# Kernel optimization log

Measured on AMD Instinct MI355X. Metric: run time of the kernel, lower is better.

Reference implementation:

```python
import jax, jax.numpy as jnp
import numpy as np

S, E, CAP = 4096, 64, 128


def setup_inputs() -> dict:
    key = jax.random.key(0)
    k1, k2 = jax.random.split(key)
    logits = jax.random.normal(k1, (S, E), dtype=jnp.float32)
    noise = jax.random.normal(k2, (S, E), dtype=jnp.float32)
    return {"logits": logits, "noise": noise, "capacity": CAP}


def reference(logits, noise, capacity):
    # logits, noise: [S, E]; capacity: python int
    gates = jax.nn.softmax(logits, axis=1)                      # [S, E]
    num_experts = gates.shape[1]

    # top-1 expert
    indices1_s = jnp.argmax(gates, axis=1)                      # [S]
    mask1 = jax.nn.one_hot(indices1_s, num_experts, dtype=jnp.int32)

    # top-2 expert from noised logits with top-1 masked out
    logits_w_noise = logits + noise
    neg_min = jnp.finfo(logits.dtype).min
    logits_except1 = jnp.where(mask1 > 0, neg_min, logits_w_noise)
    indices2_s = jnp.argmax(logits_except1, axis=1)
    mask2 = jax.nn.one_hot(indices2_s, num_experts, dtype=jnp.int32)

    # capacity locations (running count per expert over tokens)
    locations1 = jnp.cumsum(mask1, axis=0) - 1                  # [S, E]
    locations2 = jnp.cumsum(mask2, axis=0) - 1
    locations2 = locations2 + jnp.sum(mask1, axis=0, keepdims=True)

    # load-balancing aux loss
    me = jnp.mean(gates, axis=0)
    ce = jnp.mean(mask1.astype(logits.dtype), axis=0)
    l_aux = jnp.mean(me * ce) * num_experts * num_experts

    # drop tokens over capacity
    mask1 = mask1 * (locations1 < capacity).astype(mask1.dtype)
    mask2 = mask2 * (locations2 < capacity).astype(mask2.dtype)

    locations1_s = jnp.sum(locations1 * mask1, axis=1)          # [S]
    locations2_s = jnp.sum(locations2 * mask2, axis=1)

    mask1_f = mask1.astype(logits.dtype)
    mask2_f = mask2.astype(logits.dtype)
    gates1_s = jnp.einsum('se,se->s', gates, mask1_f)
    gates2_s = jnp.einsum('se,se->s', gates, mask2_f)
    denom_s = jnp.maximum(gates1_s + gates2_s, jnp.finfo(logits.dtype).eps)
    gates1_s = gates1_s / denom_s
    gates2_s = gates2_s / denom_s

    gates1 = gates1_s[:, None] * mask1_f                        # [S, E]
    gates2 = gates2_s[:, None] * mask2_f

    locations1_sc = jax.nn.one_hot(locations1_s, capacity, dtype=logits.dtype)
    locations2_sc = jax.nn.one_hot(locations2_s, capacity, dtype=logits.dtype)

    combine_weights = (gates1[:, :, None] * locations1_sc[:, None, :]
                       + gates2[:, :, None] * locations2_sc[:, None, :])  # [S, E, C]
    dispatch_mask = combine_weights.astype(bool)
    return l_aux, combine_weights, dispatch_mask
```

## Files before the change

### kernel.cpp

```cpp
#include <hip/hip_runtime.h>
#include <float.h>
#include <math.h>

#define SS 4096
#define EE 64
#define CAPC 128
#define ROW 8192
#define SEC (4096LL * 64 * 128)
#define NGATE 256
#define NFILL 4096
#define TPB_TOK 16

__global__ __launch_bounds__(256) void k1_gate_fill(
    const float* __restrict__ logits,
    const float* __restrict__ noise,
    int*   __restrict__ bc1,
    int*   __restrict__ bc2,
    float* __restrict__ pg,
    int*   __restrict__ tokmeta,
    float2* __restrict__ tokg,
    float* __restrict__ out)
{
    const int tid = threadIdx.x;

    if (blockIdx.x >= NGATE) {
        const int fb = blockIdx.x - NGATE;
        float4* p = (float4*)out + (long)fb * 4096;
        const float4 z = make_float4(0.f, 0.f, 0.f, 0.f);
        #pragma unroll
        for (int i = 0; i < 16; ++i) p[i * 256 + tid] = z;
        if (fb == NFILL - 1 && tid == 0) out[2 * SEC] = 0.f;
        return;
    }

    const int b    = blockIdx.x;
    const int wave = tid >> 6;
    const int lane = tid & 63;

    __shared__ int   s_idx1[TPB_TOK], s_idx2[TPB_TOK];
    __shared__ float s_gate[TPB_TOK][64];

    #pragma unroll
    for (int t4 = 0; t4 < 4; ++t4) {
        const int t = wave * 4 + t4;
        const int s = b * TPB_TOK + t;
        const float l = logits[s * EE + lane];
        const float n = noise [s * EE + lane];

        float v = l; int bi = lane;
        #pragma unroll
        for (int off = 32; off; off >>= 1) {
            float v2 = __shfl_xor(v, off, 64);
            int   i2 = __shfl_xor(bi, off, 64);
            if (v2 > v || (v2 == v && i2 < bi)) { v = v2; bi = i2; }
        }
        const int idx1 = bi;

        float e = expf(l - v);
        float sum = e;
        #pragma unroll
        for (int off = 32; off; off >>= 1) sum += __shfl_xor(sum, off, 64);
        const float gate = e / sum;

        float lw = (lane == idx1) ? -FLT_MAX : (l + n);
        float v2v = lw; int bi2 = lane;
        #pragma unroll
        for (int off = 32; off; off >>= 1) {
            float q  = __shfl_xor(v2v, off, 64);
            int   i2 = __shfl_xor(bi2, off, 64);
            if (q > v2v || (q == v2v && i2 < bi2)) { v2v = q; bi2 = i2; }
        }
        const int idx2 = bi2;

        s_gate[t][lane] = gate;
        const float g1v = __shfl(gate, idx1, 64);
        const float g2v = __shfl(gate, idx2, 64);
        if (lane == 0) {
            s_idx1[t] = idx1;
            s_idx2[t] = idx2;
            tokg[s] = make_float2(g1v, g2v);
        }
    }
    __syncthreads();

    if (tid < 64) {
        int c1 = 0, c2 = 0;
        float gs = 0.f;
        #pragma unroll
        for (int j = 0; j < TPB_TOK; ++j) {
            c1 += (s_idx1[j] == tid);
            c2 += (s_idx2[j] == tid);
            gs += s_gate[j][tid];
        }
        bc1[b * 64 + tid] = c1;
        bc2[b * 64 + tid] = c2;
        pg [b * 64 + tid] = gs;
    } else if (tid < 64 + TPB_TOK) {
        const int t = tid - 64;
        const int m1 = s_idx1[t], m2 = s_idx2[t];
        int r1 = 0, r2 = 0;
        for (int j = 0; j < t; ++j) {
            r1 += (s_idx1[j] == m1);
            r2 += (s_idx2[j] == m2);
        }
        tokmeta[b * TPB_TOK + t] = m1 | (m2 << 6) | (r1 << 12) | (r2 << 17);
    }
}

__global__ __launch_bounds__(256) void k2_scan_scatter(
    const int*   __restrict__ bc1,
    const int*   __restrict__ bc2,
    const float* __restrict__ pg,
    const int*   __restrict__ tokmeta,
    const float2* __restrict__ tokg,
    float* __restrict__ out)
{
    const int tid = threadIdx.x;
    const int b   = blockIdx.x;

    __shared__ int   s_off1[64], s_off2[64], s_cnt1[64];
    __shared__ float s_gs[64];

    if (tid < 64) {
        int o1 = 0, mine = 0;
        #pragma unroll 8
        for (int blk = 0; blk < NGATE; ++blk) {
            if (blk == b) mine = o1;
            o1 += bc1[blk * 64 + tid];
        }
        s_off1[tid] = mine;
        s_cnt1[tid] = o1;
    } else if (tid < 128) {
        const int e = tid - 64;
        int o2 = 0, mine = 0;
        #pragma unroll 8
        for (int blk = 0; blk < NGATE; ++blk) {
            if (blk == b) mine = o2;
            o2 += bc2[blk * 64 + e];
        }
        s_off2[e] = mine;
    } else if (tid < 192 && b == 0) {
        const int e = tid - 128;
        float gs = 0.f;
        #pragma unroll 8
        for (int blk = 0; blk < NGATE; ++blk) gs += pg[blk * 64 + e];
        s_gs[e] = gs;
    }
    __syncthreads();

    if (tid < TPB_TOK) {
        const int s = b * TPB_TOK + tid;
        const int m = tokmeta[s];
        const int i1  =  m        & 63;
        const int i2  = (m >> 6)  & 63;
        const int lr1 = (m >> 12) & 31;
        const int lr2 = (m >> 17) & 31;
        const float2 g = tokg[s];
        const int loc1 = lr1 + s_off1[i1];
        const int loc2 = lr2 + s_off2[i2] + s_cnt1[i2];
        float g1 = g.x, g2 = g.y;
        const bool k1 = loc1 < CAPC, k2 = loc2 < CAPC;
        g1 = k1 ? g1 : 0.f;
        g2 = k2 ? g2 : 0.f;
        const float denom = fmaxf(g1 + g2, 1.1920929e-07f);
        g1 /= denom;
        g2 /= denom;
        float* combine = out + 1;
        float* mask    = out + 1 + SEC;
        const long base = (long)s * ROW;
        if (k1 && g1 != 0.f) {
            const long p = base + (long)i1 * CAPC + loc1;
            combine[p] = g1;
            mask[p]    = 1.f;
        }
        if (k2 && g2 != 0.f) {
            const long p = base + (long)i2 * CAPC + loc2;
            combine[p] = g2;
            mask[p]    = 1.f;
        }
    } else if (tid == 64 + TPB_TOK && b == 0) {
        float prod = 0.f;
        #pragma unroll 8
        for (int e = 0; e < 64; ++e) prod += s_gs[e] * (float)s_cnt1[e];
        out[0] = prod * (float)EE / ((float)SS * (float)SS);
    }
}

extern "C" void kernel_launch(void* const* d_in, const int* in_sizes, int n_in,
                              void* d_out, int out_size, void* d_ws, size_t ws_size,
                              hipStream_t stream) {
    const float* logits = (const float*)d_in[0];
    const float* noise  = (const float*)d_in[1];
    float* out = (float*)d_out;

    char* ws = (char*)d_ws;
    int*    bc1     = (int*)   (ws + 0);
    int*    bc2     = (int*)   (ws + 65536);
    float*  pg      = (float*) (ws + 131072);
    int*    tokmeta = (int*)   (ws + 196608);
    float2* tokg    = (float2*)(ws + 212992);

    k1_gate_fill<<<NGATE + NFILL, 256, 0, stream>>>(logits, noise, bc1, bc2, pg,
                                                    tokmeta, tokg, out);
    k2_scan_scatter<<<NGATE, 256, 0, stream>>>(bc1, bc2, pg, tokmeta, tokg, out);
}
```

Baseline: 272.5 us.

## Fuse gating and scatter into one cooperative kernel with grid sync

```diff
diff --git a/kernel.cpp b/kernel.cpp
--- a/kernel.cpp
+++ b/kernel.cpp
@@ -1,4 +1,5 @@
 #include <hip/hip_runtime.h>
+#include <hip/hip_cooperative_groups.h>
 #include <float.h>
 #include <math.h>
 
@@ -8,118 +9,118 @@
 #define ROW 8192
 #define SEC (4096LL * 64 * 128)
 #define NGATE 256
-#define NFILL 4096
 #define TPB_TOK 16
-
-__global__ __launch_bounds__(256) void k1_gate_fill(
+#define NBLK 512
+#define F4G 28672
+#define F4F 36864
+
+namespace cg = cooperative_groups;
+
+__global__ __launch_bounds__(256, 2) void k_fused(
     const float* __restrict__ logits,
     const float* __restrict__ noise,
     int*   __restrict__ bc1,
     int*   __restrict__ bc2,
     float* __restrict__ pg,
-    int*   __restrict__ tokmeta,
-    float2* __restrict__ tokg,
-    float* __restrict__ out)
-{
-    const int tid = threadIdx.x;
-
-    if (blockIdx.x >= NGATE) {
-        const int fb = blockIdx.x - NGATE;
-        float4* p = (float4*)out + (long)fb * 4096;
-        const float4 z = make_float4(0.f, 0.f, 0.f, 0.f);
-        #pragma unroll
-        for (int i = 0; i < 16; ++i) p[i * 256 + tid] = z;
-        if (fb == NFILL - 1 && tid == 0) out[2 * SEC] = 0.f;
-        return;
-    }
-
-    const int b    = blockIdx.x;
-    const int wave = tid >> 6;
-    const int lane = tid & 63;
-
-    __shared__ int   s_idx1[TPB_TOK], s_idx2[TPB_TOK];
-    __shared__ float s_gate[TPB_TOK][64];
-
-    #pragma unroll
-    for (int t4 = 0; t4 < 4; ++t4) {
-        const int t = wave * 4 + t4;
-        const int s = b * TPB_TOK + t;
-        const float l = logits[s * EE + lane];
-        const float n = noise [s * EE + lane];
-
-        float v = l; int bi = lane;
-        #pragma unroll
-        for (int off = 32; off; off >>= 1) {
-            float v2 = __shfl_xor(v, off, 64);
-            int   i2 = __shfl_xor(bi, off, 64);
-            if (v2 > v || (v2 == v && i2 < bi)) { v = v2; bi = i2; }
-        }
-        const int idx1 = bi;
-
-        float e = expf(l - v);
-        float sum = e;
-        #pragma unroll
-        for (int off = 32; off; off >>= 1) sum += __shfl_xor(sum, off, 64);
-        const float gate = e / sum;
-
-        float lw = (lane == idx1) ? -FLT_MAX : (l + n);
-        float v2v = lw; int bi2 = lane;
-        #pragma unroll
-        for (int off = 32; off; off >>= 1) {
-            float q  = __shfl_xor(v2v, off, 64);
-            int   i2 = __shfl_xor(bi2, off, 64);
-            if (q > v2v || (q == v2v && i2 < bi2)) { v2v = q; bi2 = i2; }
-        }
-        const int idx2 = bi2;
-
-        s_gate[t][lane] = gate;
-        const float g1v = __shfl(gate, idx1, 64);
-        const float g2v = __shfl(gate, idx2, 64);
-        if (lane == 0) {
-            s_idx1[t] = idx1;
-            s_idx2[t] = idx2;
-            tokg[s] = make_float2(g1v, g2v);
-        }
-    }
-    __syncthreads();
-
-    if (tid < 64) {
-        int c1 = 0, c2 = 0;
-        float gs = 0.f;
-        #pragma unroll
-        for (int j = 0; j < TPB_TOK; ++j) {
-            c1 += (s_idx1[j] == tid);
-            c2 += (s_idx2[j] == tid);
-            gs += s_gate[j][tid];
-        }
-        bc1[b * 64 + tid] = c1;
-        bc2[b * 64 + tid] = c2;
-        pg [b * 64 + tid] = gs;
-    } else if (tid < 64 + TPB_TOK) {
-        const int t = tid - 64;
-        const int m1 = s_idx1[t], m2 = s_idx2[t];
-        int r1 = 0, r2 = 0;
-        for (int j = 0; j < t; ++j) {
-            r1 += (s_idx1[j] == m1);
-            r2 += (s_idx2[j] == m2);
-        }
-        tokmeta[b * TPB_TOK + t] = m1 | (m2 << 6) | (r1 << 12) | (r2 << 17);
-    }
-}
-
-__global__ __launch_bounds__(256) void k2_scan_scatter(
-    const int*   __restrict__ bc1,
-    const int*   __restrict__ bc2,
-    const float* __restrict__ pg,
-    const int*   __restrict__ tokmeta,
-    const float2* __restrict__ tokg,
     float* __restrict__ out)
 {
     const int tid = threadIdx.x;
     const int b   = blockIdx.x;
 
-    __shared__ int   s_off1[64], s_off2[64], s_cnt1[64];
-    __shared__ float s_gs[64];
+    __shared__ int    s_idx1[TPB_TOK], s_idx2[TPB_TOK];
+    __shared__ float  s_gate[TPB_TOK][64];
+    __shared__ int    s_meta[TPB_TOK];
+    __shared__ float2 s_g[TPB_TOK];
+    __shared__ int    s_off1[64], s_off2[64], s_cnt1[64];
+    __shared__ float  s_gs[64];
+
+    if (b < NGATE) {
+        const int wave = tid >> 6;
+        const int lane = tid & 63;
+
+        #pragma unroll
+        for (int t4 = 0; t4 < 4; ++t4) {
+            const int t = wave * 4 + t4;
+            const int s = b * TPB_TOK + t;
+            const float l = logits[s * EE + lane];
+            const float n = noise [s * EE + lane];
+
+            float v = l; int bi = lane;
+            #pragma unroll
+            for (int off = 32; off; off >>= 1) {
+                float v2 = __shfl_xor(v, off, 64);
+                int   i2 = __shfl_xor(bi, off, 64);
+                if (v2 > v || (v2 == v && i2 < bi)) { v = v2; bi = i2; }
+            }
+            const int idx1 = bi;
+
+            float e = expf(l - v);
+            float sum = e;
+            #pragma unroll
+            for (int off = 32; off; off >>= 1) sum += __shfl_xor(sum, off, 64);
+            const float gate = e / sum;
+
+            float lw = (lane == idx1) ? -FLT_MAX : (l + n);
+            float v2v = lw; int bi2 = lane;
+            #pragma unroll
+            for (int off = 32; off; off >>= 1) {
+                float q  = __shfl_xor(v2v, off, 64);
+                int   i2 = __shfl_xor(bi2, off, 64);
+                if (q > v2v || (q == v2v && i2 < bi2)) { v2v = q; bi2 = i2; }
+            }
+            const int idx2 = bi2;
+
+            s_gate[t][lane] = gate;
+            const float g1v = __shfl(gate, idx1, 64);
+            const float g2v = __shfl(gate, idx2, 64);
+            if (lane == 0) {
+                s_idx1[t] = idx1;
+                s_idx2[t] = idx2;
+                s_g[t] = make_float2(g1v, g2v);
+            }
+        }
+        __syncthreads();
+
+        if (tid < 64) {
+            int c1 = 0, c2 = 0;
+            float gs = 0.f;
+            #pragma unroll
+            for (int j = 0; j < TPB_TOK; ++j) {
+                c1 += (s_idx1[j] == tid);
+                c2 += (s_idx2[j] == tid);
+                gs += s_gate[j][tid];
+            }
+            bc1[b * 64 + tid] = c1;
+            bc2[b * 64 + tid] = c2;
+            pg [b * 64 + tid] = gs;
+        } else if (tid < 64 + TPB_TOK) {
+            const int t = tid - 64;
+            const int m1 = s_idx1[t], m2 = s_idx2[t];
+            int r1 = 0, r2 = 0;
+            for (int j = 0; j < t; ++j) {
+                r1 += (s_idx1[j] == m1);
+                r2 += (s_idx2[j] == m2);
+            }
+            s_meta[t] = m1 | (m2 << 6) | (r1 << 12) | (r2 << 17);
+        }
+    }
+
+    {
+        const float4 z = make_float4(0.f, 0.f, 0.f, 0.f);
+        if (b < NGATE) {
+            float4* p = (float4*)out + (long)b * F4G;
+            #pragma unroll 8
+            for (int i = 0; i < F4G / 256; ++i) p[i * 256 + tid] = z;
+        } else {
+            float4* p = (float4*)out + (long)NGATE * F4G + (long)(b - NGATE) * F4F;
+            #pragma unroll 8
+            for (int i = 0; i < F4F / 256; ++i) p[i * 256 + tid] = z;
+            if (b == NBLK - 1 && tid == 0) out[2 * SEC] = 0.f;
+        }
+    }
+
+    cg::this_grid().sync();
+    if (b >= NGATE) return;
 
     if (tid < 64) {
         int o1 = 0, mine = 0;
@@ -150,12 +151,12 @@
 
     if (tid < TPB_TOK) {
         const int s = b * TPB_TOK + tid;
-        const int m = tokmeta[s];
+        const int m = s_meta[tid];
         const int i1  =  m        & 63;
         const int i2  = (m >> 6)  & 63;
         const int lr1 = (m >> 12) & 31;
         const int lr2 = (m >> 17) & 31;
-        const float2 g = tokg[s];
+        const float2 g = s_g[tid];
         const int loc1 = lr1 + s_off1[i1];
         const int loc2 = lr2 + s_off2[i2] + s_cnt1[i2];
         float g1 = g.x, g2 = g.y;
@@ -194,13 +195,12 @@
     float* out = (float*)d_out;
 
     char* ws = (char*)d_ws;
-    int*    bc1     = (int*)   (ws + 0);
-    int*    bc2     = (int*)   (ws + 65536);
-    float*  pg      = (float*) (ws + 131072);
-    int*    tokmeta = (int*)   (ws + 196608);
-    float2* tokg    = (float2*)(ws + 212992);
-
-    k1_gate_fill<<<NGATE + NFILL, 256, 0, stream>>>(logits, noise, bc1, bc2, pg,
-                                                    tokmeta, tokg, out);
-    k2_scan_scatter<<<NGATE, 256, 0, stream>>>(bc1, bc2, pg, tokmeta, tokg, out);
+    int*   bc1 = (int*)  (ws + 0);
+    int*   bc2 = (int*)  (ws + 65536);
+    float* pg  = (float*)(ws + 131072);
+
+    void* args[] = { (void*)&logits, (void*)&noise, (void*)&bc1,
+                     (void*)&bc2, (void*)&pg, (void*)&out };
+    hipLaunchCooperativeKernel((void*)k_fused, dim3(NBLK), dim3(256),
+                               args, 0, stream);
 }
```

Result: slower. 356.3 us (+30.7%).

## Fuse zero-fill into per-row writer kernel with values inlined

Applied to the files above, without the earlier changes.

```diff
diff --git a/kernel.cpp b/kernel.cpp
--- a/kernel.cpp
+++ b/kernel.cpp
@@ -8,31 +8,20 @@
 #define ROW 8192
 #define SEC (4096LL * 64 * 128)
 #define NGATE 256
-#define NFILL 4096
 #define TPB_TOK 16
-
-__global__ __launch_bounds__(256) void k1_gate_fill(
+#define NW 1024
+#define TPW 4
+
+__global__ __launch_bounds__(256) void k1_gate(
     const float* __restrict__ logits,
     const float* __restrict__ noise,
     int*   __restrict__ bc1,
     int*   __restrict__ bc2,
     float* __restrict__ pg,
     int*   __restrict__ tokmeta,
-    float2* __restrict__ tokg,
-    float* __restrict__ out)
+    float2* __restrict__ tokg)
 {
-    const int tid = threadIdx.x;
-
-    if (blockIdx.x >= NGATE) {
-        const int fb = blockIdx.x - NGATE;
-        float4* p = (float4*)out + (long)fb * 4096;
-        const float4 z = make_float4(0.f, 0.f, 0.f, 0.f);
-        #pragma unroll
-        for (int i = 0; i < 16; ++i) p[i * 256 + tid] = z;
-        if (fb == NFILL - 1 && tid == 0) out[2 * SEC] = 0.f;
-        return;
-    }
-
+    const int tid  = threadIdx.x;
     const int b    = blockIdx.x;
     const int wave = tid >> 6;
     const int lane = tid & 63;
@@ -107,7 +96,32 @@
     }
 }
 
-__global__ __launch_bounds__(256) void k2_scan_scatter(
+__device__ __forceinline__ void write_row(
+    float* __restrict__ base, int p1, float v1, int p2, float v2, int tid)
+{
+    if (tid == 255) {
+        base[0]    = (p1 == 0)    ? v1 : ((p2 == 0)    ? v2 : 0.f);
+        base[1]    = (p1 == 1)    ? v1 : ((p2 == 1)    ? v2 : 0.f);
+        base[2]    = (p1 == 2)    ? v1 : ((p2 == 2)    ? v2 : 0.f);
+        base[8191] = (p1 == 8191) ? v1 : ((p2 == 8191) ? v2 : 0.f);
+    }
+    float* cbase = base + 3;
+    #pragma unroll
+    for (int j = 0; j < 8; ++j) {
+        const int k = j * 256 + tid;
+        if (j < 7 || k < 2047) {
+            const int rel = 4 * k + 3;
+            float4 z;
+            z.x = (rel + 0 == p1) ? v1 : ((rel + 0 == p2) ? v2 : 0.f);
+            z.y = (rel + 1 == p1) ? v1 : ((rel + 1 == p2) ? v2 : 0.f);
+            z.z = (rel + 2 == p1) ? v1 : ((rel + 2 == p2) ? v2 : 0.f);
+            z.w = (rel + 3 == p1) ? v1 : ((rel + 3 == p2) ? v2 : 0.f);
+            *(float4*)(cbase + 4 * (long)k) = z;
+        }
+    }
+}
+
+__global__ __launch_bounds__(256) void k2_write(
     const int*   __restrict__ bc1,
     const int*   __restrict__ bc2,
     const float* __restrict__ pg,
@@ -117,15 +131,18 @@
 {
     const int tid = threadIdx.x;
     const int b   = blockIdx.x;
+    const int gb  = b >> 2;
 
     __shared__ int   s_off1[64], s_off2[64], s_cnt1[64];
     __shared__ float s_gs[64];
+    __shared__ int   s_p1[TPW], s_p2[TPW];
+    __shared__ float s_v1[TPW], s_v2[TPW];
 
     if (tid < 64) {
         int o1 = 0, mine = 0;
         #pragma unroll 8
         for (int blk = 0; blk < NGATE; ++blk) {
-            if (blk == b) mine = o1;
+            if (blk == gb) mine = o1;
             o1 += bc1[blk * 64 + tid];
         }
         s_off1[tid] = mine;
@@ -135,7 +152,7 @@
         int o2 = 0, mine = 0;
         #pragma unroll 8
         for (int blk = 0; blk < NGATE; ++blk) {
-            if (blk == b) mine = o2;
+            if (blk == gb) mine = o2;
             o2 += bc2[blk * 64 + e];
         }
         s_off2[e] = mine;
@@ -148,8 +165,8 @@
     }
     __syncthreads();
 
-    if (tid < TPB_TOK) {
-        const int s = b * TPB_TOK + tid;
+    if (tid < TPW) {
+        const int s = b * TPW + tid;
         const int m = tokmeta[s];
         const int i1  =  m        & 63;
         const int i2  = (m >> 6)  & 63;
@@ -165,24 +182,26 @@
         const float denom = fmaxf(g1 + g2, 1.1920929e-07f);
         g1 /= denom;
         g2 /= denom;
-        float* combine = out + 1;
-        float* mask    = out + 1 + SEC;
-        const long base = (long)s * ROW;
-        if (k1 && g1 != 0.f) {
-            const long p = base + (long)i1 * CAPC + loc1;
-            combine[p] = g1;
-            mask[p]    = 1.f;
-        }
-        if (k2 && g2 != 0.f) {
-            const long p = base + (long)i2 * CAPC + loc2;
-            combine[p] = g2;
-            mask[p]    = 1.f;
-        }
-    } else if (tid == 64 + TPB_TOK && b == 0) {
+        s_p1[tid] = (k1 && g1 != 0.f) ? (i1 * CAPC + loc1) : -1;
+        s_v1[tid] = g1;
+        s_p2[tid] = (k2 && g2 != 0.f) ? (i2 * CAPC + loc2) : -1;
+        s_v2[tid] = g2;
+    } else if (tid == 192 && b == 0) {
         float prod = 0.f;
         #pragma unroll 8
         for (int e = 0; e < 64; ++e) prod += s_gs[e] * (float)s_cnt1[e];
         out[0] = prod * (float)EE / ((float)SS * (float)SS);
+    }
+    __syncthreads();
+
+    for (int t = 0; t < TPW; ++t) {
+        const int s = b * TPW + t;
+        const int p1 = s_p1[t], p2 = s_p2[t];
+        const float v1 = s_v1[t], v2 = s_v2[t];
+        float* combine = out + 1 + (long)s * ROW;
+        float* mask    = out + 1 + SEC + (long)s * ROW;
+        write_row(combine, p1, v1, p2, v2, tid);
+        write_row(mask,    p1, 1.f, p2, 1.f, tid);
     }
 }
 
@@ -200,7 +219,6 @@
     int*    tokmeta = (int*)   (ws + 196608);
     float2* tokg    = (float2*)(ws + 212992);
 
-    k1_gate_fill<<<NGATE + NFILL, 256, 0, stream>>>(logits, noise, bc1, bc2, pg,
-                                                    tokmeta, tokg, out);
-    k2_scan_scatter<<<NGATE, 256, 0, stream>>>(bc1, bc2, pg, tokmeta, tokg, out);
-}
+    k1_gate<<<NGATE, 256, 0, stream>>>(logits, noise, bc1, bc2, pg, tokmeta, tokg);
+    k2_write<<<NW, 256, 0, stream>>>(bc1, bc2, pg, tokmeta, tokg, out);
+}
```

Result: slower. 284.5 us (+4.4%).

## Fuse gating and scatter into one kernel with last-block atomic completion

Applied to the files above, without the earlier changes.

```diff
diff --git a/kernel.cpp b/kernel.cpp
--- a/kernel.cpp
+++ b/kernel.cpp
@@ -8,10 +8,11 @@
 #define ROW 8192
 #define SEC (4096LL * 64 * 128)
 #define NGATE 256
+#define TPB_TOK 16
 #define NFILL 4096
-#define TPB_TOK 16
-
-__global__ __launch_bounds__(256) void k1_gate_fill(
+#define NBLK_TOTAL (NGATE + NFILL)
+
+__global__ __launch_bounds__(256) void k_fused(
     const float* __restrict__ logits,
     const float* __restrict__ noise,
     int*   __restrict__ bc1,
@@ -19,145 +20,156 @@
     float* __restrict__ pg,
     int*   __restrict__ tokmeta,
     float2* __restrict__ tokg,
+    int*   __restrict__ ctr,
     float* __restrict__ out)
 {
     const int tid = threadIdx.x;
-
-    if (blockIdx.x >= NGATE) {
+    const int b   = blockIdx.x;
+
+    __shared__ int   s_idx1[TPB_TOK], s_idx2[TPB_TOK];
+    __shared__ float s_gate[TPB_TOK][64];
+    __shared__ int   s_part1[4][64], s_part2[4][64];
+    __shared__ int   s_c1[64];
+    __shared__ float s_gsL[64];
+    __shared__ int   s_last;
+
+    if (b >= NGATE) {
         const int fb = blockIdx.x - NGATE;
         float4* p = (float4*)out + (long)fb * 4096;
         const float4 z = make_float4(0.f, 0.f, 0.f, 0.f);
         #pragma unroll
         for (int i = 0; i < 16; ++i) p[i * 256 + tid] = z;
         if (fb == NFILL - 1 && tid == 0) out[2 * SEC] = 0.f;
-        return;
-    }
-
-    const int b    = blockIdx.x;
-    const int wave = tid >> 6;
-    const int lane = tid & 63;
-
-    __shared__ int   s_idx1[TPB_TOK], s_idx2[TPB_TOK];
-    __shared__ float s_gate[TPB_TOK][64];
-
-    #pragma unroll
-    for (int t4 = 0; t4 < 4; ++t4) {
-        const int t = wave * 4 + t4;
-        const int s = b * TPB_TOK + t;
-        const float l = logits[s * EE + lane];
-        const float n = noise [s * EE + lane];
-
-        float v = l; int bi = lane;
+    } else {
+        const int wave = tid >> 6;
+        const int lane = tid & 63;
+
         #pragma unroll
-        for (int off = 32; off; off >>= 1) {
-            float v2 = __shfl_xor(v, off, 64);
-            int   i2 = __shfl_xor(bi, off, 64);
-            if (v2 > v || (v2 == v && i2 < bi)) { v = v2; bi = i2; }
-        }
-        const int idx1 = bi;
-
-        float e = expf(l - v);
-        float sum = e;
-        #pragma unroll
-        for (int off = 32; off; off >>= 1) sum += __shfl_xor(sum, off, 64);
-        const float gate = e / sum;
-
-        float lw = (lane == idx1) ? -FLT_MAX : (l + n);
-        float v2v = lw; int bi2 = lane;
-        #pragma unroll
-        for (int off = 32; off; off >>= 1) {
-            float q  = __shfl_xor(v2v, off, 64);
-            int   i2 = __shfl_xor(bi2, off, 64);
-            if (q > v2v || (q == v2v && i2 < bi2)) { v2v = q; bi2 = i2; }
-        }
-        const int idx2 = bi2;
-
-        s_gate[t][lane] = gate;
-        const float g1v = __shfl(gate, idx1, 64);
-        const float g2v = __shfl(gate, idx2, 64);
-        if (lane == 0) {
-            s_idx1[t] = idx1;
-            s_idx2[t] = idx2;
-            tokg[s] = make_float2(g1v, g2v);
+        for (int t4 = 0; t4 < 4; ++t4) {
+            const int t = wave * 4 + t4;
+            const int s = b * TPB_TOK + t;
+            const float l = logits[s * EE + lane];
+            const float n = noise [s * EE + lane];
+
+            float v = l; int bi = lane;
+            #pragma unroll
+            for (int off = 32; off; off >>= 1) {
+                float v2 = __shfl_xor(v, off, 64);
+                int   i2 = __shfl_xor(bi, off, 64);
+                if (v2 > v || (v2 == v && i2 < bi)) { v = v2; bi = i2; }
+            }
+            const int idx1 = bi;
+
+            float e = expf(l - v);
+            float sum = e;
+            #pragma unroll
+            for (int off = 32; off; off >>= 1) sum += __shfl_xor(sum, off, 64);
+            const float gate = e / sum;
+
+            float lw = (lane == idx1) ? -FLT_MAX : (l + n);
+            float v2v = lw; int bi2 = lane;
+            #pragma unroll
+            for (int off = 32; off; off >>= 1) {
+                float q  = __shfl_xor(v2v, off, 64);
+                int   i2 = __shfl_xor(bi2, off, 64);
+                if (q > v2v || (q == v2v && i2 < bi2)) { v2v = q; bi2 = i2; }
+            }
+            const int idx2 = bi2;
+
+            s_gate[t][lane] = gate;
+            const float g1v = __shfl(gate, idx1, 64);
+            const float g2v = __shfl(gate, idx2, 64);
+            if (lane == 0) {
+                s_idx1[t] = idx1;
+                s_idx2[t] = idx2;
+                tokg[s] = make_float2(g1v, g2v);
+            }
+        }
+        __syncthreads();
+
+        if (tid < 64) {
+            int c1 = 0, c2 = 0;
+            float gs = 0.f;
+            #pragma unroll
+            for (int j = 0; j < TPB_TOK; ++j) {
+                c1 += (s_idx1[j] == tid);
+                c2 += (s_idx2[j] == tid);
+                gs += s_gate[j][tid];
+            }
+            bc1[b * 64 + tid] = c1;
+            bc2[b * 64 + tid] = c2;
+            pg [b * 64 + tid] = gs;
+        } else if (tid < 64 + TPB_TOK) {
+            const int t = tid - 64;
+            const int m1 = s_idx1[t], m2 = s_idx2[t];
+            int r1 = 0, r2 = 0;
+            for (int j = 0; j < t; ++j) {
+                r1 += (s_idx1[j] == m1);
+                r2 += (s_idx2[j] == m2);
+            }
+            tokmeta[b * TPB_TOK + t] = m1 | (m2 << 6) | (r1 << 12) | (r2 << 17);
+        }
+    }
+
+    __syncthreads();
+    if (tid == 0) {
+        __threadfence();
+        const int old = atomicAdd(ctr, 1);
+        s_last = (old == NBLK_TOTAL - 1) ? 1 : 0;
+    }
+    __syncthreads();
+    if (!s_last) return;
+    __threadfence();
+
+    const int e = tid & 63;
+    const int q = tid >> 6;
+
+    int p1 = 0, p2 = 0;
+    {
+        const int lo = q * 64, hi = lo + 64;
+        #pragma unroll 8
+        for (int blk = lo; blk < hi; ++blk) {
+            p1 += bc1[blk * 64 + e];
+            p2 += bc2[blk * 64 + e];
+        }
+        s_part1[q][e] = p1;
+        s_part2[q][e] = p2;
+    }
+    __syncthreads();
+
+    int run1 = 0, run2 = 0;
+    for (int qq = 0; qq < q; ++qq) { run1 += s_part1[qq][e]; run2 += s_part2[qq][e]; }
+    if (q == 3) s_c1[e] = run1 + p1;
+
+    {
+        const int lo = q * 64, hi = lo + 64;
+        for (int blk = lo; blk < hi; ++blk) {
+            const int v1 = bc1[blk * 64 + e]; bc1[blk * 64 + e] = run1; run1 += v1;
+            const int v2 = bc2[blk * 64 + e]; bc2[blk * 64 + e] = run2; run2 += v2;
         }
     }
     __syncthreads();
 
     if (tid < 64) {
-        int c1 = 0, c2 = 0;
-        float gs = 0.f;
-        #pragma unroll
-        for (int j = 0; j < TPB_TOK; ++j) {
-            c1 += (s_idx1[j] == tid);
-            c2 += (s_idx2[j] == tid);
-            gs += s_gate[j][tid];
-        }
-        bc1[b * 64 + tid] = c1;
-        bc2[b * 64 + tid] = c2;
-        pg [b * 64 + tid] = gs;
-    } else if (tid < 64 + TPB_TOK) {
-        const int t = tid - 64;
-        const int m1 = s_idx1[t], m2 = s_idx2[t];
-        int r1 = 0, r2 = 0;
-        for (int j = 0; j < t; ++j) {
-            r1 += (s_idx1[j] == m1);
-            r2 += (s_idx2[j] == m2);
-        }
-        tokmeta[b * TPB_TOK + t] = m1 | (m2 << 6) | (r1 << 12) | (r2 << 17);
-    }
-}
-
-__global__ __launch_bounds__(256) void k2_scan_scatter(
-    const int*   __restrict__ bc1,
-    const int*   __restrict__ bc2,
-    const float* __restrict__ pg,
-    const int*   __restrict__ tokmeta,
-    const float2* __restrict__ tokg,
-    float* __restrict__ out)
-{
-    const int tid = threadIdx.x;
-    const int b   = blockIdx.x;
-
-    __shared__ int   s_off1[64], s_off2[64], s_cnt1[64];
-    __shared__ float s_gs[64];
-
-    if (tid < 64) {
-        int o1 = 0, mine = 0;
-        #pragma unroll 8
-        for (int blk = 0; blk < NGATE; ++blk) {
-            if (blk == b) mine = o1;
-            o1 += bc1[blk * 64 + tid];
-        }
-        s_off1[tid] = mine;
-        s_cnt1[tid] = o1;
-    } else if (tid < 128) {
-        const int e = tid - 64;
-        int o2 = 0, mine = 0;
-        #pragma unroll 8
-        for (int blk = 0; blk < NGATE; ++blk) {
-            if (blk == b) mine = o2;
-            o2 += bc2[blk * 64 + e];
-        }
-        s_off2[e] = mine;
-    } else if (tid < 192 && b == 0) {
-        const int e = tid - 128;
         float gs = 0.f;
         #pragma unroll 8
-        for (int blk = 0; blk < NGATE; ++blk) gs += pg[blk * 64 + e];
-        s_gs[e] = gs;
-    }
-    __syncthreads();
-
-    if (tid < TPB_TOK) {
-        const int s = b * TPB_TOK + tid;
-        const int m = tokmeta[s];
+        for (int blk = 0; blk < NGATE; ++blk) gs += pg[blk * 64 + tid];
+        s_gsL[tid] = gs;
+    }
+
+    float* combine = out + 1;
+    float* mask    = out + 1 + SEC;
+    for (int k = 0; k < 16; ++k) {
+        const int s  = k * 256 + tid;
+        const int gb = s >> 4;
+        const int m  = tokmeta[s];
         const int i1  =  m        & 63;
         const int i2  = (m >> 6)  & 63;
         const int lr1 = (m >> 12) & 31;
         const int lr2 = (m >> 17) & 31;
         const float2 g = tokg[s];
-        const int loc1 = lr1 + s_off1[i1];
-        const int loc2 = lr2 + s_off2[i2] + s_cnt1[i2];
+        const int loc1 = lr1 + bc1[gb * 64 + i1];
+        const int loc2 = lr2 + bc2[gb * 64 + i2] + s_c1[i2];
         float g1 = g.x, g2 = g.y;
         const bool k1 = loc1 < CAPC, k2 = loc2 < CAPC;
         g1 = k1 ? g1 : 0.f;
@@ -165,8 +177,6 @@
         const float denom = fmaxf(g1 + g2, 1.1920929e-07f);
         g1 /= denom;
         g2 /= denom;
-        float* combine = out + 1;
-        float* mask    = out + 1 + SEC;
         const long base = (long)s * ROW;
         if (k1 && g1 != 0.f) {
             const long p = base + (long)i1 * CAPC + loc1;
@@ -178,10 +188,13 @@
             combine[p] = g2;
             mask[p]    = 1.f;
         }
-    } else if (tid == 64 + TPB_TOK && b == 0) {
+    }
+    __syncthreads();
+
+    if (tid == 0) {
         float prod = 0.f;
         #pragma unroll 8
-        for (int e = 0; e < 64; ++e) prod += s_gs[e] * (float)s_cnt1[e];
+        for (int ee = 0; ee < 64; ++ee) prod += s_gsL[ee] * (float)s_c1[ee];
         out[0] = prod * (float)EE / ((float)SS * (float)SS);
     }
 }
@@ -199,8 +212,9 @@
     float*  pg      = (float*) (ws + 131072);
     int*    tokmeta = (int*)   (ws + 196608);
     float2* tokg    = (float2*)(ws + 212992);
-
-    k1_gate_fill<<<NGATE + NFILL, 256, 0, stream>>>(logits, noise, bc1, bc2, pg,
-                                                    tokmeta, tokg, out);
-    k2_scan_scatter<<<NGATE, 256, 0, stream>>>(bc1, bc2, pg, tokmeta, tokg, out);
+    int*    ctr     = (int*)   (ws + 245760);
+
+    hipMemsetAsync(ctr, 0, 4, stream);
+    k_fused<<<NBLK_TOTAL, 256, 0, stream>>>(logits, noise, bc1, bc2, pg,
+                                            tokmeta, tokg, ctr, out);
 }
```

Result: slower. 458.0 us (+68.1%).
